# Kernel optimization log

Hardware: AMD Instinct MI355X
Metric: run time of the kernel (lower is better)

Reference implementation:

```python
import jax, jax.numpy as jnp
import numpy as np

D_MODEL = 512
D_INNER = 1024   # expand=2
D_STATE = 16
D_CONV = 4
DT_RANK = 32     # ceil(512/16)
SEQ = 4096
ATT_D = 128


def _mamba(x, in_w, conv_w, conv_b, xproj_w, dt_w, dt_b, A_log, Dp, out_w):
    # x: [B, L, d_model]
    B, L, _ = x.shape
    xz = x @ in_w.T                      # [B, L, 2*d_inner]
    xin, z = jnp.split(xz, 2, axis=-1)
    # depthwise causal conv1d
    xc = jnp.swapaxes(xin, 1, 2)         # [B, d_inner, L]
    xc = jax.lax.conv_general_dilated(
        xc, conv_w, (1,), [(D_CONV - 1, 0)],
        dimension_numbers=('NCH', 'OIH', 'NCH'),
        feature_group_count=D_INNER)
    xin = jax.nn.silu(jnp.swapaxes(xc + conv_b[None, :, None], 1, 2))
    # input-dependent dt, B, C
    xdbl = xin @ xproj_w.T               # [B, L, dt_rank + 2*d_state]
    dt = jax.nn.softplus(xdbl[..., :DT_RANK] @ dt_w.T + dt_b)   # [B, L, d_inner]
    Bm = xdbl[..., DT_RANK:DT_RANK + D_STATE]                   # [B, L, d_state]
    Cm = xdbl[..., DT_RANK + D_STATE:]                          # [B, L, d_state]
    A = -jnp.exp(A_log)                                          # [d_inner, d_state]
    dA = jnp.exp(dt[..., None] * A)                              # [B, L, d_inner, d_state]
    dBu = dt[..., None] * Bm[:, :, None, :] * xin[..., None]     # [B, L, d_inner, d_state]

    def step(h, t):
        a, b, c = t
        h = a * h + b                                            # [B, d_inner, d_state]
        return h, jnp.einsum('bds,bs->bd', h, c)

    h0 = jnp.zeros((B, D_INNER, D_STATE), x.dtype)
    _, ys = jax.lax.scan(step, h0,
                         (jnp.moveaxis(dA, 1, 0),
                          jnp.moveaxis(dBu, 1, 0),
                          jnp.moveaxis(Cm, 1, 0)))
    y = jnp.moveaxis(ys, 0, 1) + xin * Dp                        # [B, L, d_inner]
    return (y * jax.nn.silu(z)) @ out_w.T                        # [B, L, d_model]


def _forward(x,
             m1_in_w, m1_conv_w, m1_conv_b, m1_xproj_w, m1_dt_w, m1_dt_b, m1_A_log, m1_D, m1_out_w,
             m2_in_w, m2_conv_w, m2_conv_b, m2_xproj_w, m2_dt_w, m2_dt_b, m2_A_log, m2_D, m2_out_w,
             attn_w1, attn_b1, attn_w2, attn_b2):
    f = _mamba(x, m1_in_w, m1_conv_w, m1_conv_b, m1_xproj_w, m1_dt_w, m1_dt_b, m1_A_log, m1_D, m1_out_w)
    f = _mamba(f, m2_in_w, m2_conv_w, m2_conv_b, m2_xproj_w, m2_dt_w, m2_dt_b, m2_A_log, m2_D, m2_out_w)
    f = f[0]                                                     # [L, d_model]
    # attention-gated MIL pooling on the ORIGINAL x (as in the torch code)
    a = jnp.tanh(x[0] @ attn_w1.T + attn_b1) @ attn_w2.T + attn_b2   # [L, 1]
    a = jax.nn.softmax(a.T, axis=-1)                             # [1, L]
    return a @ f                                                 # [1, d_model]


def _mamba_params(keys, tag):
    g = lambda k, s, sc: jax.random.normal(k, s, jnp.float32) * sc
    return {
        tag + '_in_w': g(keys[0], (2 * D_INNER, D_MODEL), 0.02),
        tag + '_conv_w': g(keys[1], (D_INNER, 1, D_CONV), 0.1),
        tag + '_conv_b': jnp.zeros((D_INNER,), jnp.float32),
        tag + '_xproj_w': g(keys[2], (DT_RANK + 2 * D_STATE, D_INNER), 0.02),
        tag + '_dt_w': g(keys[3], (D_INNER, DT_RANK), 0.02),
        tag + '_dt_b': jnp.full((D_INNER,), -4.6, jnp.float32),   # softplus(-4.6) ~ 0.01
        tag + '_A_log': jnp.log(jnp.tile(jnp.arange(1, D_STATE + 1, dtype=jnp.float32), (D_INNER, 1))),
        tag + '_D': jnp.ones((D_INNER,), jnp.float32),
        tag + '_out_w': g(keys[4], (D_MODEL, D_INNER), 0.02),
    }


def setup_inputs() -> dict:
    key = jax.random.key(0)
    ks = jax.random.split(key, 16)
    inp = {'x': jax.random.normal(ks[0], (1, SEQ, D_MODEL), jnp.float32)}
    inp.update(_mamba_params(ks[1:6], 'm1'))
    inp.update(_mamba_params(ks[6:11], 'm2'))
    inp['attn_w1'] = jax.random.normal(ks[11], (ATT_D, D_MODEL), jnp.float32) * 0.05
    inp['attn_b1'] = jnp.zeros((ATT_D,), jnp.float32)
    inp['attn_w2'] = jax.random.normal(ks[12], (1, ATT_D), jnp.float32) * 0.05
    inp['attn_b2'] = jnp.zeros((1,), jnp.float32)
    return inp


def reference(x,
              m1_in_w, m1_conv_w, m1_conv_b, m1_xproj_w, m1_dt_w, m1_dt_b, m1_A_log, m1_D, m1_out_w,
              m2_in_w, m2_conv_w, m2_conv_b, m2_xproj_w, m2_dt_w, m2_dt_b, m2_A_log, m2_D, m2_out_w,
              attn_w1, attn_b1, attn_w2, attn_b2):
    return _forward(x,
                    m1_in_w, m1_conv_w, m1_conv_b, m1_xproj_w, m1_dt_w, m1_dt_b, m1_A_log, m1_D, m1_out_w,
                    m2_in_w, m2_conv_w, m2_conv_b, m2_xproj_w, m2_dt_w, m2_dt_b, m2_A_log, m2_D, m2_out_w,
                    attn_w1, attn_b1, attn_w2, attn_b2)
```

## Files before the change

kernel.cpp:

```cpp
#include <hip/hip_runtime.h>
#include <hip/hip_fp16.h>
#include <cstddef>
#include <cstdint>

#define L_SEQ   4096
#define D_MODEL 512
#define D_INNER 1024
#define D_STATE 16
#define DT_RANK 32
#define ATT_D   128
#define NCHUNK  128
#define CLEN    32

typedef __bf16 bf16;
typedef __bf16 bf16x8 __attribute__((ext_vector_type(8)));
typedef float  f32x4  __attribute__((ext_vector_type(4)));

__device__ __forceinline__ void load_lds16(const void* g, void* l) {
    __builtin_amdgcn_global_load_lds(
        (const __attribute__((address_space(1))) uint32_t*)g,
        (__attribute__((address_space(3))) uint32_t*)l, 16, 0, 0);
}

template <int NSPLIT>
__global__ void __launch_bounds__(256) gemm_bf16(const bf16* __restrict__ A,
                                                 const bf16* __restrict__ B,
                                                 float* __restrict__ C0,
                                                 float* __restrict__ C1,
                                                 float* __restrict__ C2,
                                                 int cs1, int cs2,
                                                 int ldc01, int ldc2,
                                                 int M, int N, int K) {
    constexpr int BM = 128, BN = 128, BK = 32;
    constexpr int TM = 4, TN = 4;
    __shared__ bf16 As[2][BM][BK];
    __shared__ bf16 Bs[2][BN][BK];
    const int tid  = threadIdx.x;
    const int lane = tid & 63;
    const int wid  = tid >> 6;
    const int wm   = wid >> 1;
    const int wn   = wid & 1;
    const int m_l  = lane & 15;
    const int quad = lane >> 4;

    int bx = blockIdx.x, by = blockIdx.y;
    if (gridDim.y == 32 && gridDim.x >= 16) {
        int lin = by * gridDim.x + bx;
        if (lin < 512) {
            int k = lin & 7, q = lin >> 3;
            bx = (k & 1) * 8 + (q & 7);
            by = (k >> 1) * 8 + (q >> 3);
        } else {
            bx = 16;
            by = lin - 512;
        }
    }
    const int row0 = by * BM;
    const int col0 = bx * BN;

    const int kper = K / NSPLIT;
    const int kbeg = blockIdx.z * kper;
    const int iters = kper / BK;

    f32x4 acc[TM][TN] = {};

    auto stage = [&](int k0, int buf) {
#pragma unroll
        for (int r = 0; r < 2; ++r) {
            int sl  = tid + r * 256;
            int row = sl >> 2;
            int ch  = (sl & 3) ^ ((row >> 1) & 3);
            load_lds16(A + (size_t)(row0 + row) * K + k0 + ch * 8,
                       (char*)&As[buf][0][0] + sl * 16);
        }
#pragma unroll
        for (int r = 0; r < 2; ++r) {
            int sl  = tid + r * 256;
            int row = sl >> 2;
            int ch  = (sl & 3) ^ ((row >> 1) & 3);
            load_lds16(B + (size_t)(col0 + row) * K + k0 + ch * 8,
                       (char*)&Bs[buf][0][0] + sl * 16);
        }
    };

    stage(kbeg, 0);
    for (int it = 0; it < iters; ++it) {
        int cur = it & 1;
        __syncthreads();
        if (it + 1 < iters) stage(kbeg + (it + 1) * BK, cur ^ 1);

        bf16x8 af[TM], bfr[TN];
#pragma unroll
        for (int i = 0; i < TM; ++i) {
            int r = wm * 64 + i * 16 + m_l;
            af[i] = *(const bf16x8*)&As[cur][r][(quad ^ ((r >> 1) & 3)) * 8];
        }
#pragma unroll
        for (int j = 0; j < TN; ++j) {
            int r = wn * 64 + j * 16 + m_l;
            bfr[j] = *(const bf16x8*)&Bs[cur][r][(quad ^ ((r >> 1) & 3)) * 8];
        }
#pragma unroll
        for (int i = 0; i < TM; ++i)
#pragma unroll
            for (int j = 0; j < TN; ++j)
                acc[i][j] = __builtin_amdgcn_mfma_f32_16x16x32_bf16(
                                af[i], bfr[j], acc[i][j], 0, 0, 0);
    }
#pragma unroll
    for (int i = 0; i < TM; ++i)
#pragma unroll
        for (int j = 0; j < TN; ++j) {
            int rr = row0 + wm * 64 + i * 16 + quad * 4;
            int cc = col0 + wn * 64 + j * 16 + m_l;
            float* base; int c2; int ld;
            if (cc < cs1)      { base = C0; c2 = cc;       ld = ldc01; }
            else if (cc < cs2) { base = C1; c2 = cc - cs1; ld = ldc01; }
            else               { base = C2; c2 = cc - cs2; ld = ldc2; }
            base += (size_t)blockIdx.z * (size_t)M * ld;
#pragma unroll
            for (int g = 0; g < 4; ++g)
                base[(size_t)(rr + g) * ld + c2] = acc[i][j][g];
        }
}

#define N_INW  (2048 * 512)
#define N_OUTW (512 * 1024)
#define N_X    (4096 * 512)
#define N_ATTW (128 * 512)

__global__ void split_all_k(const float* __restrict__ in_w0, const float* __restrict__ out_w0,
                            const float* __restrict__ in_w1, const float* __restrict__ out_w1,
                            const float* __restrict__ x, const float* __restrict__ attn_w1,
                            bf16* __restrict__ Win0, bf16* __restrict__ Wout0,
                            bf16* __restrict__ Win1, bf16* __restrict__ Wout1,
                            bf16* __restrict__ Ax) {
    int i = blockIdx.x * 256 + threadIdx.x;
    const float* src; bf16* dst; int K; int act = 0;
    if (i < N_INW)                  { src = in_w0;  dst = Win0;  K = 512; }
    else if ((i -= N_INW) < N_OUTW) { src = out_w0; dst = Wout0; K = 1024; }
    else if ((i -= N_OUTW) < N_INW) { src = in_w1;  dst = Win1;  K = 512; }
    else if ((i -= N_INW) < N_OUTW) { src = out_w1; dst = Wout1; K = 1024; }
    else if ((i -= N_OUTW) < N_X)   { src = x;      dst = Ax;    K = 512; act = 1; }
    else if ((i -= N_X) < N_ATTW)   { src = attn_w1; dst = Win0 + (size_t)2048 * 1024; K = 512; }
    else return;
    int row = i / K, col = i - row * K;
    float v = src[i];
    bf16 h = (bf16)v;
    bf16* yr = dst + (size_t)row * 2 * K;
    if (act) {
        bf16 l = (bf16)(v - (float)h);
        yr[col] = h; yr[K + col] = l;
    } else {
        yr[col] = h; yr[K + col] = h;
    }
}

__global__ void __launch_bounds__(256) xdbl_conv_sgemm(
        const float* __restrict__ XIN, const float* __restrict__ cw,
        const float* __restrict__ cb, const float* __restrict__ xproj,
        float* __restrict__ U, float* __restrict__ XDBLP) {
    constexpr int BK = 16;
    __shared__ float As[BK][64 + 4];
    __shared__ float Bs[BK][64 + 4];
    const int tid = threadIdx.x;
    const int tx = tid & 15;
    const int ty = tid >> 4;
    const int row0 = blockIdx.y * 64;
    const int kbeg = blockIdx.z * 128;
    float* Cz = XDBLP + (size_t)blockIdx.z * L_SEQ * 64;

    const int m  = tid >> 2;
    const int kk = (tid & 3) << 2;
    const int t  = row0 + m;

    float acc[4][4] = {};

    for (int k0 = kbeg; k0 < kbeg + 128; k0 += BK) {
        {
            int d = k0 + kk;
            float4 a4 = *(const float4*)(cb + d);
            float cwa[4][4];
            *(float4*)cwa[0] = *(const float4*)(cw + (size_t)(d + 0) * 4);
            *(float4*)cwa[1] = *(const float4*)(cw + (size_t)(d + 1) * 4);
            *(float4*)cwa[2] = *(const float4*)(cw + (size_t)(d + 2) * 4);
            *(float4*)cwa[3] = *(const float4*)(cw + (size_t)(d + 3) * 4);
#pragma unroll
            for (int j = 0; j < 4; ++j) {
                int tt = t - 3 + j;
                if (tt >= 0) {
                    float4 xv = *(const float4*)(XIN + (size_t)tt * D_INNER + d);
                    a4.x = fmaf(cwa[0][j], xv.x, a4.x);
                    a4.y = fmaf(cwa[1][j], xv.y, a4.y);
                    a4.z = fmaf(cwa[2][j], xv.z, a4.z);
                    a4.w = fmaf(cwa[3][j], xv.w, a4.w);
                }
            }
            a4.x = a4.x / (1.f + __expf(-a4.x));
            a4.y = a4.y / (1.f + __expf(-a4.y));
            a4.z = a4.z / (1.f + __expf(-a4.z));
            a4.w = a4.w / (1.f + __expf(-a4.w));
            As[kk + 0][m] = a4.x; As[kk + 1][m] = a4.y;
            As[kk + 2][m] = a4.z; As[kk + 3][m] = a4.w;
            *(float4*)(U + (size_t)t * D_INNER + d) = a4;
        }
        {
            float4 v = *(const float4*)(xproj + (size_t)m * D_INNER + k0 + kk);
            Bs[kk + 0][m] = v.x; Bs[kk + 1][m] = v.y;
            Bs[kk + 2][m] = v.z; Bs[kk + 3][m] = v.w;
        }
        __syncthreads();
#pragma unroll
        for (int k = 0; k < BK; ++k) {
            float a[4], b[4];
#pragma unroll
            for (int i = 0; i < 4; ++i) a[i] = As[k][ty * 4 + i];
#pragma unroll
            for (int j = 0; j < 4; ++j) b[j] = Bs[k][tx * 4 + j];
#pragma unroll
            for (int i = 0; i < 4; ++i)
#pragma unroll
                for (int j = 0; j < 4; ++j)
                    acc[i][j] = fmaf(a[i], b[j], acc[i][j]);
        }
        __syncthreads();
    }
#pragma unroll
    for (int i = 0; i < 4; ++i) {
        size_t r = (size_t)(row0 + ty * 4 + i);
#pragma unroll
        for (int j = 0; j < 4; ++j)
            Cz[r * 64 + tx * 4 + j] = acc[i][j];
    }
}

__device__ __forceinline__ float softplus_f(float v) {
    return (v > 20.f) ? v : log1pf(__expf(v));
}

__global__ void __launch_bounds__(256) dtv_reduce_k(
        const float* __restrict__ XDBLP, const float* __restrict__ dt_w,
        const float* __restrict__ dtb, float* __restrict__ XDBL,
        __half* __restrict__ DTV) {
    const int t0 = blockIdx.x * 16;
    __shared__ float sx[16][32];
#pragma unroll
    for (int e = 0; e < 4; ++e) {
        int idx = threadIdx.x + e * 256;
        int r = idx >> 6, c = idx & 63;
        float v = 0.f;
#pragma unroll
        for (int s = 0; s < 8; ++s)
            v += XDBLP[(size_t)s * (L_SEQ * 64) + (size_t)(t0 + r) * 64 + c];
        if (blockIdx.y == 0) XDBL[(size_t)(t0 + r) * 64 + c] = v;
        if (c < 32) sx[r][c] = v;
    }
    __syncthreads();
    const int d = blockIdx.y * 256 + threadIdx.x;
    float wdt[32];
#pragma unroll
    for (int q = 0; q < 8; ++q) {
        float4 v = *(const float4*)(dt_w + (size_t)d * 32 + q * 4);
        wdt[q*4+0] = v.x; wdt[q*4+1] = v.y; wdt[q*4+2] = v.z; wdt[q*4+3] = v.w;
    }
    const float bias = dtb[d];
    for (int r = 0; r < 16; ++r) {
        const float4* xr = (const float4*)&sx[r][0];
        float dot = bias;
#pragma unroll
        for (int q = 0; q < 8; ++q) {
            float4 v = xr[q];
            dot = fmaf(v.x, wdt[q*4+0], dot); dot = fmaf(v.y, wdt[q*4+1], dot);
            dot = fmaf(v.z, wdt[q*4+2], dot); dot = fmaf(v.w, wdt[q*4+3], dot);
        }
        DTV[(size_t)(t0 + r) * D_INNER + d] = __float2half(softplus_f(dot));
    }
}

__global__ void reduce_aug_k(const float* __restrict__ Pp, float* __restrict__ Y,
                             bf16* __restrict__ Aaug, int n, int nslab) {
    int i = blockIdx.x * 256 + threadIdx.x;
    if (i >= n) return;
    float v = 0.f;
    for (int k = 0; k < nslab; ++k) v += Pp[(size_t)k * n + i];
    if (Y) Y[i] = v;
    if (Aaug) {
        int row = i >> 9, col = i & 511;
        bf16 h = (bf16)v;
        bf16 l = (bf16)(v - (float)h);
        bf16* r = Aaug + (size_t)row * 1024;
        r[col] = h; r[512 + col] = l;
    }
}

__device__ __forceinline__ void pow_tree(float r, float* dA) {
    float r2 = r * r, r4 = r2 * r2, r8 = r4 * r4;
    dA[0] = r;        dA[1] = r2;       dA[2] = r2 * r;   dA[3] = r4;
    dA[4] = r4 * r;   dA[5] = r4 * r2;  dA[6] = r4 * dA[2]; dA[7] = r8;
    dA[8] = r8 * r;   dA[9] = r8 * r2;  dA[10] = r8 * dA[2]; dA[11] = r8 * r4;
    dA[12] = r8 * dA[4]; dA[13] = r8 * dA[5]; dA[14] = r8 * dA[6]; dA[15] = r8 * r8;
}

__global__ void __launch_bounds__(256) scan_pass1(
        const float* __restrict__ U, const float* __restrict__ XDBL,
        const __half* __restrict__ DTV, const float* __restrict__ A_log,
        float* __restrict__ P, float* __restrict__ HLOC) {
    const int d = blockIdx.y * 256 + threadIdx.x;
    const int c = blockIdx.x;
    const float Ac0 = -__expf(A_log[(size_t)d * 16]);
    float h[16] = {};
    float sumdt = 0.f;

    const int t0 = c * CLEN;
    for (int i = 0; i < CLEN; ++i) {
        int t = t0 + i;
        const float4* xr = (const float4*)(XDBL + (size_t)t * 64);
        float dtv = __half2float(DTV[(size_t)t * D_INNER + d]);
        sumdt += dtv;
        float uu  = U[(size_t)t * D_INNER + d];
        float duu = dtv * uu;
        float4 B0 = xr[8], B1 = xr[9], B2 = xr[10], B3 = xr[11];
        float Bv[16] = {B0.x,B0.y,B0.z,B0.w, B1.x,B1.y,B1.z,B1.w,
                        B2.x,B2.y,B2.z,B2.w, B3.x,B3.y,B3.z,B3.w};
        float dA[16];
        pow_tree(__expf(dtv * Ac0), dA);
#pragma unroll
        for (int s = 0; s < 16; ++s)
            h[s] = fmaf(dA[s], h[s], duu * Bv[s]);
    }
    float Pp[16];
    pow_tree(__expf(Ac0 * sumdt), Pp);
#pragma unroll
    for (int s = 0; s < 16; ++s) {
        size_t idx = (size_t)c * (D_INNER * D_STATE) + s * D_INNER + d;
        P[idx] = Pp[s];
        HLOC[idx] = h[s];
    }
}

__global__ void __launch_bounds__(256) scan_pass2(const float* __restrict__ P,
                                                  float* HLOC) {
    const int gl  = threadIdx.x & 63;
    const int seg = threadIdx.x >> 6;
    const int g   = blockIdx.x * 64 + gl;
    const int STRIDE = D_INNER * D_STATE;
    const int c0 = seg * 32;

    float h = 0.f, q = 1.f;
    for (int c = c0; c < c0 + 32; ++c) {
        float p = P[(size_t)c * STRIDE + g];
        h = fmaf(p, h, HLOC[(size_t)c * STRIDE + g]);
        q *= p;
    }
    __shared__ float shQ[4][64];
    __shared__ float shH[4][64];
    shQ[seg][gl] = q;
    shH[seg][gl] = h;
    __syncthreads();
    float hin = 0.f;
    for (int k = 0; k < seg; ++k)
        hin = fmaf(shQ[k][gl], hin, shH[k][gl]);
    for (int c = c0; c < c0 + 32; ++c) {
        float p  = P[(size_t)c * STRIDE + g];
        float hl = HLOC[(size_t)c * STRIDE + g];
        float tmp = fmaf(p, hin, hl);
        HLOC[(size_t)c * STRIDE + g] = hin;
        hin = tmp;
    }
}

__global__ void __launch_bounds__(256) scan_pass3(
        const float* __restrict__ U, const float* __restrict__ XDBL,
        const __half* __restrict__ DTV, const float* __restrict__ A_log,
        const float* __restrict__ Dp, const float* __restrict__ Z,
        const float* __restrict__ HIN, bf16* __restrict__ Aaug) {
    const int d = blockIdx.y * 256 + threadIdx.x;
    const int c = blockIdx.x;
    const float Ac0 = -__expf(A_log[(size_t)d * 16]);
    const float Dv = Dp[d];
    float h[16];
#pragma unroll
    for (int s = 0; s < 16; ++s)
        h[s] = HIN[(size_t)c * (D_INNER * D_STATE) + s * D_INNER + d];

    const int t0 = c * CLEN;
    for (int i = 0; i < CLEN; ++i) {
        int t = t0 + i;
        const float4* xr = (const float4*)(XDBL + (size_t)t * 64);
        float dtv = __half2float(DTV[(size_t)t * D_INNER + d]);
        float uu  = U[(size_t)t * D_INNER + d];
        float duu = dtv * uu;
        float4 B0 = xr[8],  B1 = xr[9],  B2 = xr[10], B3 = xr[11];
        float4 C0 = xr[12], C1 = xr[13], C2 = xr[14], C3 = xr[15];
        float Bv[16] = {B0.x,B0.y,B0.z,B0.w, B1.x,B1.y,B1.z,B1.w,
                        B2.x,B2.y,B2.z,B2.w, B3.x,B3.y,B3.z,B3.w};
        float Cv[16] = {C0.x,C0.y,C0.z,C0.w, C1.x,C1.y,C1.z,C1.w,
                        C2.x,C2.y,C2.z,C2.w, C3.x,C3.y,C3.z,C3.w};
        float dA[16];
        pow_tree(__expf(dtv * Ac0), dA);
        float p = 0.f;
#pragma unroll
        for (int s = 0; s < 16; ++s) {
            h[s] = fmaf(dA[s], h[s], duu * Bv[s]);
            p = fmaf(h[s], Cv[s], p);
        }
        float y = fmaf(uu, Dv, p);
        float z = Z[(size_t)t * D_INNER + d];
        float sz = z / (1.f + __expf(-z));
        float g = y * sz;
        bf16 hi = (bf16)g;
        bf16 lo = (bf16)(g - (float)hi);
        bf16* row = Aaug + (size_t)t * 2048;
        row[d] = hi; row[1024 + d] = lo;
    }
}

__global__ void __launch_bounds__(256) attn_logits_exp(
        const float* __restrict__ ha, const float* __restrict__ b1,
        const float* __restrict__ w2, const float* __restrict__ b2,
        float* __restrict__ E, float* __restrict__ Sp) {
    const int j    = threadIdx.x & 127;
    const int half = threadIdx.x >> 7;
    const int t    = blockIdx.x * 2 + half;
    float hv = ha[(size_t)t * ATT_D + j];
    float v = tanhf(hv + b1[j]) * w2[j];
#pragma unroll
    for (int off = 32; off > 0; off >>= 1) v += __shfl_down(v, off, 64);
    __shared__ float sh[4];
    const int wid = threadIdx.x >> 6;
    if ((threadIdx.x & 63) == 0) sh[wid] = v;
    __syncthreads();
    if (threadIdx.x == 0) {
        float e0 = __expf(sh[0] + sh[1] + b2[0]);
        float e1 = __expf(sh[2] + sh[3] + b2[0]);
        E[t] = e0;
        E[t + 1] = e1;
        Sp[blockIdx.x] = e0 + e1;
    }
}

__global__ void weighted_sum(const float* __restrict__ E, const float* __restrict__ Sp,
                             const float* __restrict__ f, float* __restrict__ out) {
    __shared__ float ssum[256];
    int tid = threadIdx.x;
    float s = 0.f;
    for (int i = tid; i < 2048; i += 256) s += Sp[i];
    ssum[tid] = s;
    __syncthreads();
    for (int st = 128; st > 0; st >>= 1) {
        if (tid < st) ssum[tid] += ssum[tid + st];
        __syncthreads();
    }
    float S = ssum[0];
    int jl = tid & 63, tq = tid >> 6;
    int j = blockIdx.x * 64 + jl;
    float acc = 0.f;
    int tbase = blockIdx.y * 512 + tq * 128;
    for (int i = 0; i < 128; ++i) {
        int t = tbase + i;
        acc = fmaf(E[t], f[(size_t)t * D_MODEL + j], acc);
    }
    __shared__ float sred[4][64];
    sred[tq][jl] = acc;
    __syncthreads();
    if (tq == 0)
        atomicAdd(&out[j], (sred[0][jl] + sred[1][jl] + sred[2][jl] + sred[3][jl]) / S);
}

extern "C" void kernel_launch(void* const* d_in, const int* in_sizes, int n_in,
                              void* d_out, int out_size, void* d_ws, size_t ws_size,
                              hipStream_t stream) {
    (void)in_sizes; (void)n_in; (void)out_size; (void)ws_size;
    const float* x = (const float*)d_in[0];
    const float* m_in_w[2]   = {(const float*)d_in[1],  (const float*)d_in[10]};
    const float* m_conv_w[2] = {(const float*)d_in[2],  (const float*)d_in[11]};
    const float* m_conv_b[2] = {(const float*)d_in[3],  (const float*)d_in[12]};
    const float* m_xproj[2]  = {(const float*)d_in[4],  (const float*)d_in[13]};
    const float* m_dt_w[2]   = {(const float*)d_in[5],  (const float*)d_in[14]};
    const float* m_dt_b[2]   = {(const float*)d_in[6],  (const float*)d_in[15]};
    const float* m_A_log[2]  = {(const float*)d_in[7],  (const float*)d_in[16]};
    const float* m_D[2]      = {(const float*)d_in[8],  (const float*)d_in[17]};
    const float* m_out_w[2]  = {(const float*)d_in[9],  (const float*)d_in[18]};
    const float* attn_w1 = (const float*)d_in[19];
    const float* attn_b1 = (const float*)d_in[20];
    const float* attn_w2 = (const float*)d_in[21];
    const float* attn_b2 = (const float*)d_in[22];

    const int L = L_SEQ;
    float* ws = (float*)d_ws;
    float* XIN   = ws;
    float* AUXA  = XIN  + (size_t)L * 1024;
    float* Z     = AUXA + 2097152;
    float* U     = Z    + (size_t)L * 1024;
    float* XDBL  = U    + (size_t)L * 1024;
    float* FREG  = XDBL + (size_t)L * 64;
    float* W1i   = FREG + 3145728;
    float* W1o   = W1i  + 1671168;
    float* W2i   = W1o  + 786432;
    float* W2o   = W2i  + 1572864;
    float* P     = W2o  + 786432;
    float* HLOC  = P    + (size_t)NCHUNK * D_INNER * D_STATE;
    float* HA    = HLOC + (size_t)NCHUNK * D_INNER * D_STATE;
    float* Sp    = HA   + (size_t)L * ATT_D;

    bf16* AaugOut = (bf16*)XIN;
    bf16* AaugIn  = (bf16*)FREG;
    __half* DTV   = (__half*)FREG;
    bf16* WaugIn[2]  = {(bf16*)W1i, (bf16*)W2i};
    bf16* WaugOut[2] = {(bf16*)W1o, (bf16*)W2o};
    float* XDBLP = P;
    float* OutP  = Z;
    float* F2    = FREG;
    float* E     = FREG + 2097152;

    split_all_k<<<(2 * N_INW + 2 * N_OUTW + N_X + N_ATTW) / 256, 256, 0, stream>>>(
        m_in_w[0], m_out_w[0], m_in_w[1], m_out_w[1], x, attn_w1,
        WaugIn[0], WaugOut[0], WaugIn[1], WaugOut[1], AaugIn);

    auto mamba = [&](int b, float* FoutY, bf16* FoutAug) {
        if (b == 0)
            gemm_bf16<1><<<dim3(17, 32, 1), 256, 0, stream>>>(
                AaugIn, WaugIn[0], XIN, Z, HA, 1024, 2048, 1024, ATT_D, L, 2176, 1024);
        else
            gemm_bf16<1><<<dim3(16, 32, 1), 256, 0, stream>>>(
                AaugIn, WaugIn[1], XIN, Z, nullptr, 1024, 2048, 1024, 0, L, 2048, 1024);
        xdbl_conv_sgemm<<<dim3(1, L / 64, 8), 256, 0, stream>>>(
            XIN, m_conv_w[b], m_conv_b[b], m_xproj[b], U, XDBLP);
        dtv_reduce_k<<<dim3(L / 16, 4), 256, 0, stream>>>(
            XDBLP, m_dt_w[b], m_dt_b[b], XDBL, DTV);
        scan_pass1<<<dim3(NCHUNK, 4), 256, 0, stream>>>(
            U, XDBL, DTV, m_A_log[b], P, HLOC);
        scan_pass2<<<(D_INNER * D_STATE) / 64, 256, 0, stream>>>(P, HLOC);
        scan_pass3<<<dim3(NCHUNK, 4), 256, 0, stream>>>(
            U, XDBL, DTV, m_A_log[b], m_D[b], Z, HLOC, AaugOut);
        gemm_bf16<4><<<dim3(4, 32, 4), 256, 0, stream>>>(
            AaugOut, WaugOut[b], OutP, nullptr, nullptr, 512, 512, 512, 0, L, 512, 2048);
        reduce_aug_k<<<(L * 512 + 255) / 256, 256, 0, stream>>>(OutP, FoutY, FoutAug, L * 512, 4);
    };

    mamba(0, nullptr, AaugIn);
    mamba(1, F2, nullptr);

    attn_logits_exp<<<L / 2, 256, 0, stream>>>(HA, attn_b1, attn_w2, attn_b2, E, Sp);
    hipMemsetAsync(d_out, 0, D_MODEL * sizeof(float), stream);
    weighted_sum<<<dim3(D_MODEL / 64, 8), 256, 0, stream>>>(E, Sp, F2, (float*)d_out);
}
```

Before: 406.3 us.

## Compute local scan output in pass1 and apply carry-in correction in pass3

Restructures the chunked selective scan. Pass1 now produces the local output y (with zero initial state) and the running decay product per timestep, stored as fp16, so pass3 no longer repeats the 16-state recurrence. Pass3 only adds the linear correction C·(q^s)·h_in. Pass2 stores only one decay value per channel and chunk and rebuilds powers on the fly, which cuts the P traffic. The cost is extra fp16 writes and reads of YL and QC, and some precision loss from storing the cumulative decay and local output in fp16.

```diff
diff --git a/kernel.cpp b/kernel.cpp
--- a/kernel.cpp
+++ b/kernel.cpp
@@ -304,84 +304,15 @@
 __global__ void __launch_bounds__(256) scan_pass1(
         const float* __restrict__ U, const float* __restrict__ XDBL,
         const __half* __restrict__ DTV, const float* __restrict__ A_log,
-        float* __restrict__ P, float* __restrict__ HLOC) {
-    const int d = blockIdx.y * 256 + threadIdx.x;
-    const int c = blockIdx.x;
-    const float Ac0 = -__expf(A_log[(size_t)d * 16]);
-    float h[16] = {};
-    float sumdt = 0.f;
-
-    const int t0 = c * CLEN;
-    for (int i = 0; i < CLEN; ++i) {
-        int t = t0 + i;
-        const float4* xr = (const float4*)(XDBL + (size_t)t * 64);
-        float dtv = __half2float(DTV[(size_t)t * D_INNER + d]);
-        sumdt += dtv;
-        float uu  = U[(size_t)t * D_INNER + d];
-        float duu = dtv * uu;
-        float4 B0 = xr[8], B1 = xr[9], B2 = xr[10], B3 = xr[11];
-        float Bv[16] = {B0.x,B0.y,B0.z,B0.w, B1.x,B1.y,B1.z,B1.w,
-                        B2.x,B2.y,B2.z,B2.w, B3.x,B3.y,B3.z,B3.w};
-        float dA[16];
-        pow_tree(__expf(dtv * Ac0), dA);
-#pragma unroll
-        for (int s = 0; s < 16; ++s)
-            h[s] = fmaf(dA[s], h[s], duu * Bv[s]);
-    }
-    float Pp[16];
-    pow_tree(__expf(Ac0 * sumdt), Pp);
-#pragma unroll
-    for (int s = 0; s < 16; ++s) {
-        size_t idx = (size_t)c * (D_INNER * D_STATE) + s * D_INNER + d;
-        P[idx] = Pp[s];
-        HLOC[idx] = h[s];
-    }
-}
-
-__global__ void __launch_bounds__(256) scan_pass2(const float* __restrict__ P,
-                                                  float* HLOC) {
-    const int gl  = threadIdx.x & 63;
-    const int seg = threadIdx.x >> 6;
-    const int g   = blockIdx.x * 64 + gl;
-    const int STRIDE = D_INNER * D_STATE;
-    const int c0 = seg * 32;
-
-    float h = 0.f, q = 1.f;
-    for (int c = c0; c < c0 + 32; ++c) {
-        float p = P[(size_t)c * STRIDE + g];
-        h = fmaf(p, h, HLOC[(size_t)c * STRIDE + g]);
-        q *= p;
-    }
-    __shared__ float shQ[4][64];
-    __shared__ float shH[4][64];
-    shQ[seg][gl] = q;
-    shH[seg][gl] = h;
-    __syncthreads();
-    float hin = 0.f;
-    for (int k = 0; k < seg; ++k)
-        hin = fmaf(shQ[k][gl], hin, shH[k][gl]);
-    for (int c = c0; c < c0 + 32; ++c) {
-        float p  = P[(size_t)c * STRIDE + g];
-        float hl = HLOC[(size_t)c * STRIDE + g];
-        float tmp = fmaf(p, hin, hl);
-        HLOC[(size_t)c * STRIDE + g] = hin;
-        hin = tmp;
-    }
-}
-
-__global__ void __launch_bounds__(256) scan_pass3(
-        const float* __restrict__ U, const float* __restrict__ XDBL,
-        const __half* __restrict__ DTV, const float* __restrict__ A_log,
-        const float* __restrict__ Dp, const float* __restrict__ Z,
-        const float* __restrict__ HIN, bf16* __restrict__ Aaug) {
+        const float* __restrict__ Dp,
+        float* __restrict__ P0, float* __restrict__ HLOC,
+        __half* __restrict__ YL, __half* __restrict__ QC) {
     const int d = blockIdx.y * 256 + threadIdx.x;
     const int c = blockIdx.x;
     const float Ac0 = -__expf(A_log[(size_t)d * 16]);
     const float Dv = Dp[d];
-    float h[16];
-#pragma unroll
-    for (int s = 0; s < 16; ++s)
-        h[s] = HIN[(size_t)c * (D_INNER * D_STATE) + s * D_INNER + d];
+    float h[16] = {};
+    float qrun = 1.f;
 
     const int t0 = c * CLEN;
     for (int i = 0; i < CLEN; ++i) {
@@ -397,14 +328,95 @@
         float Cv[16] = {C0.x,C0.y,C0.z,C0.w, C1.x,C1.y,C1.z,C1.w,
                         C2.x,C2.y,C2.z,C2.w, C3.x,C3.y,C3.z,C3.w};
         float dA[16];
-        pow_tree(__expf(dtv * Ac0), dA);
+        float r = __expf(dtv * Ac0);
+        pow_tree(r, dA);
+        qrun *= r;
         float p = 0.f;
 #pragma unroll
         for (int s = 0; s < 16; ++s) {
             h[s] = fmaf(dA[s], h[s], duu * Bv[s]);
             p = fmaf(h[s], Cv[s], p);
         }
-        float y = fmaf(uu, Dv, p);
+        YL[(size_t)t * D_INNER + d] = __float2half(fmaf(uu, Dv, p));
+        QC[(size_t)t * D_INNER + d] = __float2half(qrun);
+    }
+    P0[(size_t)c * D_INNER + d] = qrun;
+#pragma unroll
+    for (int s = 0; s < 16; ++s)
+        HLOC[(size_t)c * (D_INNER * D_STATE) + s * D_INNER + d] = h[s];
+}
+
+__global__ void __launch_bounds__(256) scan_pass2(const float* __restrict__ P0,
+                                                  float* HLOC) {
+    const int gl  = threadIdx.x & 63;
+    const int seg = threadIdx.x >> 6;
+    const int g   = blockIdx.x * 64 + gl;
+    const int s   = g >> 10;
+    const int e   = s + 1;
+    const int d   = g & 1023;
+    const int STRIDE = D_INNER * D_STATE;
+    const int c0 = seg * 32;
+
+    auto powe = [&](float p) {
+        float p2 = p * p, p4 = p2 * p2, p8 = p4 * p4;
+        float q = 1.f;
+        if (e & 1)  q *= p;
+        if (e & 2)  q *= p2;
+        if (e & 4)  q *= p4;
+        if (e & 8)  q *= p8;
+        if (e & 16) q *= p8 * p8;
+        return q;
+    };
+
+    float h = 0.f, pr = 1.f;
+    for (int c = c0; c < c0 + 32; ++c) {
+        float p = powe(P0[(size_t)c * D_INNER + d]);
+        h = fmaf(p, h, HLOC[(size_t)c * STRIDE + g]);
+        pr *= p;
+    }
+    __shared__ float shQ[4][64];
+    __shared__ float shH[4][64];
+    shQ[seg][gl] = pr;
+    shH[seg][gl] = h;
+    __syncthreads();
+    float hin = 0.f;
+    for (int k = 0; k < seg; ++k)
+        hin = fmaf(shQ[k][gl], hin, shH[k][gl]);
+    for (int c = c0; c < c0 + 32; ++c) {
+        float p  = powe(P0[(size_t)c * D_INNER + d]);
+        float hl = HLOC[(size_t)c * STRIDE + g];
+        float tmp = fmaf(p, hin, hl);
+        HLOC[(size_t)c * STRIDE + g] = hin;
+        hin = tmp;
+    }
+}
+
+__global__ void __launch_bounds__(256) scan_pass3(
+        const float* __restrict__ XDBL, const __half* __restrict__ YL,
+        const __half* __restrict__ QC, const float* __restrict__ Z,
+        const float* __restrict__ HIN, bf16* __restrict__ Aaug) {
+    const int d = blockIdx.y * 256 + threadIdx.x;
+    const int c = blockIdx.x;
+    float hin[16];
+#pragma unroll
+    for (int s = 0; s < 16; ++s)
+        hin[s] = HIN[(size_t)c * (D_INNER * D_STATE) + s * D_INNER + d];
+
+    const int t0 = c * CLEN;
+    for (int i = 0; i < CLEN; ++i) {
+        int t = t0 + i;
+        const float4* xr = (const float4*)(XDBL + (size_t)t * 64);
+        float4 C0 = xr[12], C1 = xr[13], C2 = xr[14], C3 = xr[15];
+        float Cv[16] = {C0.x,C0.y,C0.z,C0.w, C1.x,C1.y,C1.z,C1.w,
+                        C2.x,C2.y,C2.z,C2.w, C3.x,C3.y,C3.z,C3.w};
+        float q = __half2float(QC[(size_t)t * D_INNER + d]);
+        float qa[16];
+        pow_tree(q, qa);
+        float corr = 0.f;
+#pragma unroll
+        for (int s = 0; s < 16; ++s)
+            corr = fmaf(Cv[s] * qa[s], hin[s], corr);
+        float y = __half2float(YL[(size_t)t * D_INNER + d]) + corr;
         float z = Z[(size_t)t * D_INNER + d];
         float sz = z / (1.f + __expf(-z));
         float g = y * sz;
@@ -502,10 +514,13 @@
     float* HLOC  = P    + (size_t)NCHUNK * D_INNER * D_STATE;
     float* HA    = HLOC + (size_t)NCHUNK * D_INNER * D_STATE;
     float* Sp    = HA   + (size_t)L * ATT_D;
+    float* P0    = Sp   + 2048;
 
     bf16* AaugOut = (bf16*)XIN;
     bf16* AaugIn  = (bf16*)FREG;
     __half* DTV   = (__half*)FREG;
+    __half* YL    = (__half*)AUXA;
+    __half* QC    = (__half*)P;
     bf16* WaugIn[2]  = {(bf16*)W1i, (bf16*)W2i};
     bf16* WaugOut[2] = {(bf16*)W1o, (bf16*)W2o};
     float* XDBLP = P;
@@ -529,10 +544,10 @@
         dtv_reduce_k<<<dim3(L / 16, 4), 256, 0, stream>>>(
             XDBLP, m_dt_w[b], m_dt_b[b], XDBL, DTV);
         scan_pass1<<<dim3(NCHUNK, 4), 256, 0, stream>>>(
-            U, XDBL, DTV, m_A_log[b], P, HLOC);
-        scan_pass2<<<(D_INNER * D_STATE) / 64, 256, 0, stream>>>(P, HLOC);
+            U, XDBL, DTV, m_A_log[b], m_D[b], P0, HLOC, YL, QC);
+        scan_pass2<<<(D_INNER * D_STATE) / 64, 256, 0, stream>>>(P0, HLOC);
         scan_pass3<<<dim3(NCHUNK, 4), 256, 0, stream>>>(
-            U, XDBL, DTV, m_A_log[b], m_D[b], Z, HLOC, AaugOut);
+            XDBL, YL, QC, Z, HLOC, AaugOut);
         gemm_bf16<4><<<dim3(4, 32, 4), 256, 0, stream>>>(
             AaugOut, WaugOut[b], OutP, nullptr, nullptr, 512, 512, 512, 0, L, 512, 2048);
         reduce_aug_k<<<(L * 512 + 255) / 256, 256, 0, stream>>>(OutP, FoutY, FoutAug, L * 512, 4);
```

After: 424.7 us. +4.5%, slower.
